# Kernel tuning notes

Measured on AMD Instinct MI355X. Metric: run time of the kernel, lower is better.

Reference implementation:

```python
import jax, jax.numpy as jnp
import numpy as np

B, L, D, H = 2, 2048, 1024, 16
NUM_BUCKETS, MAX_DISTANCE = 32, 128


def _rel_pos_buckets(qlen, klen, num_buckets, max_distance):
    """T5-style bidirectional relative position bucketing. Returns [qlen, klen] int32."""
    ctx = jnp.arange(qlen, dtype=jnp.int32)[:, None]
    mem = jnp.arange(klen, dtype=jnp.int32)[None, :]
    rel = mem - ctx  # memory_position - context_position
    nb = num_buckets // 2
    buckets = (rel > 0).astype(jnp.int32) * nb
    n = jnp.abs(rel)
    max_exact = nb // 2
    is_small = n < max_exact
    nf = jnp.maximum(n.astype(jnp.float32), 1.0)
    large = max_exact + (
        jnp.log(nf / max_exact) / np.float32(np.log(max_distance / max_exact)) * (nb - max_exact)
    ).astype(jnp.int32)
    large = jnp.minimum(large, nb - 1)
    return buckets + jnp.where(is_small, n, large)


def setup_inputs() -> dict:
    key = jax.random.key(0)
    ks = jax.random.split(key, 11)
    s = 0.02
    return {
        "x": jax.random.normal(ks[0], (B, L, D), dtype=jnp.float32),
        "mask": jax.random.randint(ks[1], (B, 1, L, L), 0, 2, dtype=jnp.int32),
        "Wq_w": jax.random.normal(ks[2], (D, D), dtype=jnp.float32) * s,
        "Wq_b": jnp.zeros((D,), dtype=jnp.float32),
        "Wk_w": jax.random.normal(ks[3], (D, D), dtype=jnp.float32) * s,
        "Wk_b": jnp.zeros((D,), dtype=jnp.float32),
        "Wv_w": jax.random.normal(ks[4], (D, D), dtype=jnp.float32) * s,
        "Wv_b": jnp.zeros((D,), dtype=jnp.float32),
        "Wo_w": jax.random.normal(ks[5], (D, D), dtype=jnp.float32) * s,
        "Wo_b": jnp.zeros((D,), dtype=jnp.float32),
        "rel_emb": jax.random.normal(ks[6], (NUM_BUCKETS, H), dtype=jnp.float32) * s,
    }


def reference(x, mask, Wq_w, Wq_b, Wk_w, Wk_b, Wv_w, Wv_b, Wo_w, Wo_b, rel_emb):
    b, l, d = x.shape
    h = H
    dk = d // h
    # torch Linear: y = x @ W.T + b
    Q = (x @ Wq_w.T + Wq_b).reshape(b, l, h, dk)
    K = (x @ Wk_w.T + Wk_b).reshape(b, l, h, dk)
    V = (x @ Wv_w.T + Wv_b).reshape(b, l, h, dk)
    scores = jnp.einsum("bqhd,bkhd->bhqk", Q, K) / jnp.sqrt(jnp.float32(dk))
    buckets = _rel_pos_buckets(l, l, NUM_BUCKETS, MAX_DISTANCE)  # [L, L]
    bias = rel_emb[buckets]  # [L, L, H]
    scores = scores + jnp.transpose(bias, (2, 0, 1))[None]  # [1, H, L, L]
    scores = jnp.where(mask == 0, jnp.float32(-1e9), scores)
    attn = jax.nn.softmax(scores, axis=-1)
    out = jnp.einsum("bhqk,bkhd->bqhd", attn, V).reshape(b, l, d)
    return out @ Wo_w.T + Wo_b
```

## Files before the change

kernel.cpp:

```cpp
#include <hip/hip_runtime.h>
#include <hip/hip_fp16.h>

#define B_ 2
#define L_ 2048
#define D_ 1024
#define H_ 16

typedef __attribute__((ext_vector_type(8))) _Float16 f16x8;
typedef __attribute__((ext_vector_type(4))) _Float16 f16x4;
typedef __attribute__((ext_vector_type(2))) __fp16 fp16x2;
typedef __attribute__((ext_vector_type(4))) float f32x4;

#define LOG2E 1.44269504088896f

__device__ __forceinline__ void gload_lds16(const void* g, void* l) {
  __builtin_amdgcn_global_load_lds(
      (const __attribute__((address_space(1))) unsigned int*)g,
      (__attribute__((address_space(3))) unsigned int*)l, 16, 0, 0);
}

__global__ __launch_bounds__(256) void cvt_all(
    const float* __restrict__ x, const float* __restrict__ Wq,
    const float* __restrict__ Wk, const float* __restrict__ Wv,
    const float* __restrict__ Wo, __half* __restrict__ xh,
    __half* __restrict__ wqh, __half* __restrict__ wkh,
    __half* __restrict__ wvh, __half* __restrict__ woh) {
  int i = blockIdx.x * 256 + threadIdx.x;
  const float* src;
  __half* dst;
  int j;
  if (i < 1048576) {
    src = x; dst = xh; j = i;
  } else {
    int k = i - 1048576;
    int wsel = k >> 18;
    j = k & 262143;
    src = wsel == 0 ? Wq : (wsel == 1 ? Wk : (wsel == 2 ? Wv : Wo));
    dst = wsel == 0 ? wqh : (wsel == 1 ? wkh : (wsel == 2 ? wvh : woh));
  }
  float4 v = ((const float4*)src)[j];
  __half2* o = (__half2*)(dst + (size_t)j * 4);
  o[0] = __floats2half2_rn(v.x, v.y);
  o[1] = __floats2half2_rn(v.z, v.w);
}

__global__ __launch_bounds__(256) void pack_mask(const int* __restrict__ m,
                                                 unsigned long long* __restrict__ bits) {
  int wword = blockIdx.x * 4 + (threadIdx.x >> 6);
  int lane = threadIdx.x & 63;
  int v = m[(size_t)wword * 64 + lane];
  unsigned long long bal = __ballot(v != 0);
  if (lane == 0) bits[wword] = bal;
}

__global__ __launch_bounds__(256) void bias_table(const float* __restrict__ rel_emb,
                                                  float* __restrict__ tab) {
  int i = blockIdx.x * 256 + threadIdx.x;
  if (i >= H_ * 4095) return;
  int h = i / 4095, idx = i - h * 4095;
  int rel = idx - 2047;
  int n = rel < 0 ? -rel : rel;
  int bkt;
  if (n < 8) {
    bkt = n;
  } else {
    float t = logf((float)n / 8.0f) / 2.772588722239781f * 8.0f;
    int v = 8 + (int)t;
    bkt = v < 15 ? v : 15;
  }
  if (rel > 0) bkt += 16;
  tab[i] = rel_emb[bkt * H_ + h] * LOG2E;
}

template <bool CT>
__device__ __forceinline__ void gemm_tile(const __half* __restrict__ A,
                                          const __half* __restrict__ Bw,
                                          int m0, int n0,
                                          __half* sA, __half* sB,
                                          f32x4 (&acc)[4][4],
                                          int lane, int wm, int wn, int t) {
  for (int k0 = 0; k0 < 1024; k0 += 64) {
    __syncthreads();
#pragma unroll
    for (int it = 0; it < 4; ++it) {
      int c = t + it * 256;
      int row = c >> 3, seg = c & 7;
      gload_lds16(A + ((size_t)(m0 + row) << 10) + k0 + seg * 8, sA + c * 8);
      gload_lds16(Bw + ((size_t)(n0 + row) << 10) + k0 + seg * 8, sB + c * 8);
    }
    __syncthreads();
#pragma unroll
    for (int kk = 0; kk < 2; ++kk) {
      const int off = kk * 32 + (lane >> 4) * 8;
      const int rr = lane & 15;
      f16x8 af[4], bf[4];
#pragma unroll
      for (int i = 0; i < 4; ++i) af[i] = *(const f16x8*)&sA[(wm * 64 + i * 16 + rr) * 64 + off];
#pragma unroll
      for (int i = 0; i < 4; ++i) bf[i] = *(const f16x8*)&sB[(wn * 64 + i * 16 + rr) * 64 + off];
#pragma unroll
      for (int mi = 0; mi < 4; ++mi)
#pragma unroll
        for (int ni = 0; ni < 4; ++ni) {
          if (CT)
            acc[mi][ni] = __builtin_amdgcn_mfma_f32_16x16x32_f16(bf[ni], af[mi], acc[mi][ni], 0, 0, 0);
          else
            acc[mi][ni] = __builtin_amdgcn_mfma_f32_16x16x32_f16(af[mi], bf[ni], acc[mi][ni], 0, 0, 0);
        }
    }
  }
}

__global__ __launch_bounds__(256) void gemm_qkv(
    const __half* __restrict__ xh,
    const __half* __restrict__ Wq, const __half* __restrict__ Wk, const __half* __restrict__ Wv,
    const float* __restrict__ bq, const float* __restrict__ bk, const float* __restrict__ bvv,
    __half* __restrict__ Qh, __half* __restrict__ Kh, __half* __restrict__ Vt) {
  __shared__ __align__(16) __half sA[128 * 64];
  __shared__ __align__(16) __half sB[128 * 64];
  const int m0 = blockIdx.x * 128;
  const int ng = blockIdx.y * 128;
  const int widx = ng >> 10;
  const int n0 = ng & 1023;
  const __half* Bw = widx == 0 ? Wq : (widx == 1 ? Wk : Wv);
  const float* bias = widx == 0 ? bq : (widx == 1 ? bk : bvv);
  const int t = threadIdx.x, lane = t & 63, w = t >> 6;
  const int wm = w >> 1, wn = w & 1;
  const int lg = lane >> 4, lr = lane & 15;
  f32x4 acc[4][4] = {};
  if (widx == 2) {
    gemm_tile<false>(xh, Bw, m0, n0, sA, sB, acc, lane, wm, wn, t);
#pragma unroll
    for (int mi = 0; mi < 4; ++mi)
#pragma unroll
      for (int ni = 0; ni < 4; ++ni) {
        int m = m0 + wm * 64 + mi * 16 + lg * 4;
        int n = n0 + wn * 64 + ni * 16 + lr;
        float bvx = bias[n];
        int b = m >> 11, l = m & 2047, hh = n >> 6, dd = n & 63;
        f32x4 a = acc[mi][ni];
        size_t base = ((size_t)((b * 16 + hh) * 64 + dd)) * 2048 + l;
        __half2 p0 = __floats2half2_rn(a.x + bvx, a.y + bvx);
        __half2 p1 = __floats2half2_rn(a.z + bvx, a.w + bvx);
        *(__half2*)(Vt + base) = p0;
        *(__half2*)(Vt + base + 2) = p1;
      }
  } else {
    gemm_tile<true>(xh, Bw, m0, n0, sA, sB, acc, lane, wm, wn, t);
    __half* dst = widx == 0 ? Qh : Kh;
    const float scf = widx == 0 ? 0.125f * LOG2E : 1.0f;
#pragma unroll
    for (int mi = 0; mi < 4; ++mi)
#pragma unroll
      for (int ni = 0; ni < 4; ++ni) {
        int m = m0 + wm * 64 + mi * 16 + lr;
        int n = n0 + wn * 64 + ni * 16 + 4 * lg;
        f32x4 bb = *(const f32x4*)&bias[n];
        int b = m >> 11, l = m & 2047, hh = n >> 6, dd = n & 63;
        f16x4 ov;
#pragma unroll
        for (int r = 0; r < 4; ++r) ov[r] = (_Float16)((acc[mi][ni][r] + bb[r]) * scf);
        *(f16x4*)(dst + (((size_t)(b * 16 + hh)) * 2048 + l) * 64 + dd) = ov;
      }
  }
}

__global__ __launch_bounds__(256) void gemm_out(
    const __half* __restrict__ AO, const __half* __restrict__ Wo,
    const float* __restrict__ bo, float* __restrict__ out) {
  __shared__ __align__(16) __half sA[128 * 64];
  __shared__ __align__(16) __half sB[128 * 64];
  const int m0 = blockIdx.x * 128;
  const int n0 = blockIdx.y * 128;
  const int t = threadIdx.x, lane = t & 63, w = t >> 6;
  const int wm = w >> 1, wn = w & 1;
  const int lg = lane >> 4, lr = lane & 15;
  f32x4 acc[4][4] = {};
  gemm_tile<true>(AO, Wo, m0, n0, sA, sB, acc, lane, wm, wn, t);
#pragma unroll
  for (int mi = 0; mi < 4; ++mi)
#pragma unroll
    for (int ni = 0; ni < 4; ++ni) {
      int m = m0 + wm * 64 + mi * 16 + lr;
      int n = n0 + wn * 64 + ni * 16 + 4 * lg;
      f32x4 bb = *(const f32x4*)&bo[n];
      f32x4 vv;
#pragma unroll
      for (int r = 0; r < 4; ++r) vv[r] = acc[mi][ni][r] + bb[r];
      *(f32x4*)(out + (size_t)m * 1024 + n) = vv;
    }
}

__global__ __launch_bounds__(256, 4) void attn(
    const __half* __restrict__ Qh, const __half* __restrict__ Kh,
    const __half* __restrict__ Vt, const unsigned long long* __restrict__ mb64,
    const float* __restrict__ tab, __half* __restrict__ AO) {
  const int id = blockIdx.x;
  const int ii = id >> 3;
  const int bh = (id & 7) * 4 + (ii >> 5);
  const int q0 = (ii & 31) * 64;
  const int b = bh >> 4, h = bh & 15;
  const int t = threadIdx.x, lane = t & 63, w = t >> 6;
  const int lg = lane >> 4, lr = lane & 15;

  __shared__ __align__(16) __half sK[2][64 * 64];
  __shared__ __align__(16) __half sV[2][64 * 64];
  __shared__ float sbias[260];
  __shared__ __align__(8) __half lutm[16][4];

  for (int i = t; i < 257; i += 256) sbias[i] = tab[h * 4095 + 1919 + i];
  if (t < 64) {
    int e = t >> 2, j = t & 3;
    lutm[e][j] = ((e >> j) & 1) ? __half(1.0f) : __half(0.0f);
  }

  const size_t bh2048 = (size_t)bh * 2048;
  const int qrow = q0 + w * 16 + lr;
  const __half* qp = Qh + (bh2048 + qrow) * 64 + lg * 8;
  f16x8 aq0 = *(const f16x8*)qp;
  f16x8 aq1 = *(const f16x8*)(qp + 32);

  const __half* Kb = Kh + bh2048 * 64;
  const __half* Vb = Vt + bh2048 * 64;
  const unsigned long long* mrow = mb64 + ((size_t)(b * 2048 + qrow)) * 32;

  f32x4 o[4] = {};
  f32x4 osum = {};
  unsigned long long mw = mrow[0];
  const f16x4 ones = {(_Float16)1.f, (_Float16)1.f, (_Float16)1.f, (_Float16)1.f};

#pragma unroll
  for (int it = 0; it < 2; ++it) {
    int c = t + it * 256;
    int row = c >> 3, seg = c & 7;
    int gs = (seg ^ row) & 7;
    gload_lds16(Kb + ((size_t)row << 6) + gs * 8, &sK[0][c * 8]);
    gload_lds16(Vb + ((size_t)row << 11) + gs * 8, &sV[0][c * 8]);
  }
  __syncthreads();
  const float c_neg = sbias[0], c_pos = sbias[256];

  for (int k0 = 0; k0 < L_; k0 += 64) {
    const int cur = (k0 >> 6) & 1, nxt = cur ^ 1;
    if (k0 + 64 < L_) {
#pragma unroll
      for (int it = 0; it < 2; ++it) {
        int c = t + it * 256;
        int row = c >> 3, seg = c & 7;
        int gs = (seg ^ row) & 7;
        gload_lds16(Kb + ((size_t)(k0 + 64 + row) << 6) + gs * 8, &sK[nxt][c * 8]);
        gload_lds16(Vb + ((size_t)row << 11) + (k0 + 64) + gs * 8, &sV[nxt][c * 8]);
      }
    }
    unsigned long long mw_nxt = (k0 + 64 < L_) ? mrow[(k0 >> 6) + 1] : 0;

    __builtin_amdgcn_s_setprio(1);
    f32x4 s[4] = {};
#pragma unroll
    for (int ct = 0; ct < 4; ++ct) {
      int row = ct * 16 + lr;
      const __half* rb = &sK[cur][row * 64];
      f16x8 kf0 = *(const f16x8*)(rb + ((8 * lg) ^ ((row & 7) << 3)));
      f16x8 kf1 = *(const f16x8*)(rb + ((32 + 8 * lg) ^ ((row & 7) << 3)));
      s[ct] = __builtin_amdgcn_mfma_f32_16x16x32_f16(kf0, aq0, s[ct], 0, 0, 0);
      s[ct] = __builtin_amdgcn_mfma_f32_16x16x32_f16(kf1, aq1, s[ct], 0, 0, 0);
    }
    __builtin_amdgcn_s_setprio(0);

    const int diff = k0 - q0 - w * 16;
    if (diff >= 143) {
#pragma unroll
      for (int ct = 0; ct < 4; ++ct)
#pragma unroll
        for (int r = 0; r < 4; ++r) s[ct][r] += c_pos;
    } else if (diff <= -191) {
#pragma unroll
      for (int ct = 0; ct < 4; ++ct)
#pragma unroll
        for (int r = 0; r < 4; ++r) s[ct][r] += c_neg;
    } else {
      const int ibase = diff + 4 * lg - lr + 128;
#pragma unroll
      for (int ct = 0; ct < 4; ++ct)
#pragma unroll
        for (int r = 0; r < 4; ++r) {
          int idx = ibase + 16 * ct + r;
          idx = idx < 0 ? 0 : (idx > 256 ? 256 : idx);
          s[ct][r] += sbias[idx];
        }
    }

    f16x4 pa[4];
#pragma unroll
    for (int ct = 0; ct < 4; ++ct) {
      unsigned bits = (unsigned)(mw >> (16 * ct + 4 * lg)) & 15u;
      const __half2* lm = (const __half2*)&lutm[bits][0];
      __half2 m01 = lm[0], m23 = lm[1];
      fp16x2 p01 = __builtin_amdgcn_cvt_pkrtz(exp2f(s[ct][0]), exp2f(s[ct][1]));
      fp16x2 p23 = __builtin_amdgcn_cvt_pkrtz(exp2f(s[ct][2]), exp2f(s[ct][3]));
      f16x4 pc;
      ((__half2*)&pc)[0] = __hmul2(*(__half2*)&p01, m01);
      ((__half2*)&pc)[1] = __hmul2(*(__half2*)&p23, m23);
      pa[ct] = pc;
    }

    __builtin_amdgcn_s_setprio(1);
#pragma unroll
    for (int ct = 0; ct < 4; ++ct) {
      osum = __builtin_amdgcn_mfma_f32_16x16x16f16(ones, pa[ct], osum, 0, 0, 0);
#pragma unroll
      for (int dt = 0; dt < 4; ++dt) {
        int row = dt * 16 + lr;
        const __half* vp = &sV[cur][row * 64 + ((16 * ct + 4 * lg) ^ ((row & 7) << 3))];
        f16x4 bv = *(const f16x4*)vp;
        o[dt] = __builtin_amdgcn_mfma_f32_16x16x16f16(bv, pa[ct], o[dt], 0, 0, 0);
      }
    }
    __builtin_amdgcn_s_setprio(0);
    __syncthreads();
    mw = mw_nxt;
  }
  const float rl = 1.0f / osum[0];
  const size_t qbase = ((size_t)(b * L_ + q0 + w * 16 + lr)) * D_ + h * 64;
#pragma unroll
  for (int dt = 0; dt < 4; ++dt) {
    f16x4 ov;
#pragma unroll
    for (int r = 0; r < 4; ++r) ov[r] = (_Float16)(o[dt][r] * rl);
    *(f16x4*)(AO + qbase + dt * 16 + 4 * lg) = ov;
  }
}

extern "C" void kernel_launch(void* const* d_in, const int* in_sizes, int n_in,
                              void* d_out, int out_size, void* d_ws, size_t ws_size,
                              hipStream_t stream) {
  const float* x = (const float*)d_in[0];
  const int* mask = (const int*)d_in[1];
  const float* Wq_w = (const float*)d_in[2];
  const float* Wq_b = (const float*)d_in[3];
  const float* Wk_w = (const float*)d_in[4];
  const float* Wk_b = (const float*)d_in[5];
  const float* Wv_w = (const float*)d_in[6];
  const float* Wv_b = (const float*)d_in[7];
  const float* Wo_w = (const float*)d_in[8];
  const float* Wo_b = (const float*)d_in[9];
  const float* rel_emb = (const float*)d_in[10];
  float* out = (float*)d_out;

  char* ws = (char*)d_ws;
  const size_t MB = 1024 * 1024;
  __half* xh = (__half*)(ws);
  __half* wqh = (__half*)(ws + 8 * MB);
  __half* wkh = (__half*)(ws + 10 * MB);
  __half* wvh = (__half*)(ws + 12 * MB);
  __half* woh = (__half*)(ws + 14 * MB);
  __half* Qh = (__half*)(ws + 16 * MB);
  __half* Kh = (__half*)(ws + 24 * MB);
  __half* Vt = (__half*)(ws + 32 * MB);
  unsigned long long* mb64 = (unsigned long long*)(ws + 40 * MB);
  float* tab = (float*)(ws + 48 * MB);
  __half* AO = xh;

  cvt_all<<<8192, 256, 0, stream>>>(x, Wq_w, Wk_w, Wv_w, Wo_w, xh, wqh, wkh, wvh, woh);
  pack_mask<<<32768, 256, 0, stream>>>(mask, mb64);
  bias_table<<<256, 256, 0, stream>>>(rel_emb, tab);

  gemm_qkv<<<dim3(32, 24), 256, 0, stream>>>(xh, wqh, wkh, wvh, Wq_b, Wk_b, Wv_b, Qh, Kh, Vt);
  attn<<<1024, 256, 0, stream>>>(Qh, Kh, Vt, mb64, tab, AO);
  gemm_out<<<dim3(32, 8), 256, 0, stream>>>(AO, woh, Wo_b, out);
}
```

Baseline: 182.6 us.

## Enlarge attention blocks to 128 queries and remap GEMM blocks per XCD

The attention kernel now runs 512-thread blocks covering 128 query rows, so each K/V tile staged in shared memory is shared by eight waves instead of four and the number of K/V loads is halved. V fragments are loaded into registers ahead of the softmax so their LDS latency overlaps the exp work. Both GEMMs switch to a 1D grid with an XCD-aware block mapping that keeps blocks sharing the same M rows on one XCD for L2 locality. The cost is higher register pressure from the preloaded V fragments and fewer, larger attention blocks, which can lower occupancy.

```diff
diff --git a/kernel.cpp b/kernel.cpp
--- a/kernel.cpp
+++ b/kernel.cpp
@@ -118,8 +118,10 @@
     __half* __restrict__ Qh, __half* __restrict__ Kh, __half* __restrict__ Vt) {
   __shared__ __align__(16) __half sA[128 * 64];
   __shared__ __align__(16) __half sB[128 * 64];
-  const int m0 = blockIdx.x * 128;
-  const int ng = blockIdx.y * 128;
+  const int lin = blockIdx.x;
+  const int xcd = lin & 7, idx = lin >> 3;
+  const int m0 = (xcd * 4 + (idx & 3)) * 128;
+  const int ng = (idx >> 2) * 128;
   const int widx = ng >> 10;
   const int n0 = ng & 1023;
   const __half* Bw = widx == 0 ? Wq : (widx == 1 ? Wk : Wv);
@@ -170,8 +172,10 @@
     const float* __restrict__ bo, float* __restrict__ out) {
   __shared__ __align__(16) __half sA[128 * 64];
   __shared__ __align__(16) __half sB[128 * 64];
-  const int m0 = blockIdx.x * 128;
-  const int n0 = blockIdx.y * 128;
+  const int lin = blockIdx.x;
+  const int xcd = lin & 7, idx = lin >> 3;
+  const int m0 = (xcd * 4 + (idx & 3)) * 128;
+  const int n0 = (idx >> 2) * 128;
   const int t = threadIdx.x, lane = t & 63, w = t >> 6;
   const int wm = w >> 1, wn = w & 1;
   const int lg = lane >> 4, lr = lane & 15;
@@ -191,14 +195,14 @@
     }
 }
 
-__global__ __launch_bounds__(256, 4) void attn(
+__global__ __launch_bounds__(512, 4) void attn(
     const __half* __restrict__ Qh, const __half* __restrict__ Kh,
     const __half* __restrict__ Vt, const unsigned long long* __restrict__ mb64,
     const float* __restrict__ tab, __half* __restrict__ AO) {
   const int id = blockIdx.x;
   const int ii = id >> 3;
-  const int bh = (id & 7) * 4 + (ii >> 5);
-  const int q0 = (ii & 31) * 64;
+  const int bh = (id & 7) * 4 + (ii >> 4);
+  const int q0 = (ii & 15) * 128;
   const int b = bh >> 4, h = bh & 15;
   const int t = threadIdx.x, lane = t & 63, w = t >> 6;
   const int lg = lane >> 4, lr = lane & 15;
@@ -208,7 +212,7 @@
   __shared__ float sbias[260];
   __shared__ __align__(8) __half lutm[16][4];
 
-  for (int i = t; i < 257; i += 256) sbias[i] = tab[h * 4095 + 1919 + i];
+  for (int i = t; i < 257; i += 512) sbias[i] = tab[h * 4095 + 1919 + i];
   if (t < 64) {
     int e = t >> 2, j = t & 3;
     lutm[e][j] = ((e >> j) & 1) ? __half(1.0f) : __half(0.0f);
@@ -229,9 +233,8 @@
   unsigned long long mw = mrow[0];
   const f16x4 ones = {(_Float16)1.f, (_Float16)1.f, (_Float16)1.f, (_Float16)1.f};
 
-#pragma unroll
-  for (int it = 0; it < 2; ++it) {
-    int c = t + it * 256;
+  {
+    int c = t;
     int row = c >> 3, seg = c & 7;
     int gs = (seg ^ row) & 7;
     gload_lds16(Kb + ((size_t)row << 6) + gs * 8, &sK[0][c * 8]);
@@ -243,14 +246,11 @@
   for (int k0 = 0; k0 < L_; k0 += 64) {
     const int cur = (k0 >> 6) & 1, nxt = cur ^ 1;
     if (k0 + 64 < L_) {
-#pragma unroll
-      for (int it = 0; it < 2; ++it) {
-        int c = t + it * 256;
-        int row = c >> 3, seg = c & 7;
-        int gs = (seg ^ row) & 7;
-        gload_lds16(Kb + ((size_t)(k0 + 64 + row) << 6) + gs * 8, &sK[nxt][c * 8]);
-        gload_lds16(Vb + ((size_t)row << 11) + (k0 + 64) + gs * 8, &sV[nxt][c * 8]);
-      }
+      int c = t;
+      int row = c >> 3, seg = c & 7;
+      int gs = (seg ^ row) & 7;
+      gload_lds16(Kb + ((size_t)(k0 + 64 + row) << 6) + gs * 8, &sK[nxt][c * 8]);
+      gload_lds16(Vb + ((size_t)row << 11) + (k0 + 64) + gs * 8, &sV[nxt][c * 8]);
     }
     unsigned long long mw_nxt = (k0 + 64 < L_) ? mrow[(k0 >> 6) + 1] : 0;
 
@@ -266,6 +266,15 @@
       s[ct] = __builtin_amdgcn_mfma_f32_16x16x32_f16(kf1, aq1, s[ct], 0, 0, 0);
     }
     __builtin_amdgcn_s_setprio(0);
+
+    f16x4 bv[4][4];
+#pragma unroll
+    for (int ct = 0; ct < 4; ++ct)
+#pragma unroll
+      for (int dt = 0; dt < 4; ++dt) {
+        int row = dt * 16 + lr;
+        bv[ct][dt] = *(const f16x4*)&sV[cur][row * 64 + ((16 * ct + 4 * lg) ^ ((row & 7) << 3))];
+      }
 
     const int diff = k0 - q0 - w * 16;
     if (diff >= 143) {
@@ -309,12 +318,8 @@
     for (int ct = 0; ct < 4; ++ct) {
       osum = __builtin_amdgcn_mfma_f32_16x16x16f16(ones, pa[ct], osum, 0, 0, 0);
 #pragma unroll
-      for (int dt = 0; dt < 4; ++dt) {
-        int row = dt * 16 + lr;
-        const __half* vp = &sV[cur][row * 64 + ((16 * ct + 4 * lg) ^ ((row & 7) << 3))];
-        f16x4 bv = *(const f16x4*)vp;
-        o[dt] = __builtin_amdgcn_mfma_f32_16x16x16f16(bv, pa[ct], o[dt], 0, 0, 0);
-      }
+      for (int dt = 0; dt < 4; ++dt)
+        o[dt] = __builtin_amdgcn_mfma_f32_16x16x16f16(bv[ct][dt], pa[ct], o[dt], 0, 0, 0);
     }
     __builtin_amdgcn_s_setprio(0);
     __syncthreads();
@@ -365,7 +370,7 @@
   pack_mask<<<32768, 256, 0, stream>>>(mask, mb64);
   bias_table<<<256, 256, 0, stream>>>(rel_emb, tab);
 
-  gemm_qkv<<<dim3(32, 24), 256, 0, stream>>>(xh, wqh, wkh, wvh, Wq_b, Wk_b, Wv_b, Qh, Kh, Vt);
-  attn<<<1024, 256, 0, stream>>>(Qh, Kh, Vt, mb64, tab, AO);
-  gemm_out<<<dim3(32, 8), 256, 0, stream>>>(AO, woh, Wo_b, out);
-}
+  gemm_qkv<<<768, 256, 0, stream>>>(xh, wqh, wkh, wvh, Wq_b, Wk_b, Wv_b, Qh, Kh, Vt);
+  attn<<<512, 512, 0, stream>>>(Qh, Kh, Vt, mb64, tab, AO);
+  gemm_out<<<256, 256, 0, stream>>>(AO, woh, Wo_b, out);
+}
```

Result: slower. 188.6 us (+3.3%).
